# Kernel optimization log

Hardware: AMD Instinct MI355X
Metric: run time of the kernel (lower is better)

## Reference

```python
import jax, jax.numpy as jnp
import numpy as np

NUM_EMBEDDINGS = 1024
EMBEDDING_DIM = 128
COMMITMENT_COST = 0.25


def setup_inputs() -> dict:
    key = jax.random.key(0)
    k_in, k_cb = jax.random.split(key)
    inputs = jax.random.normal(k_in, (65536, EMBEDDING_DIM), dtype=jnp.float32)
    # torch init: uniform(-1/K, 1/K)
    codebook = jax.random.uniform(
        k_cb, (NUM_EMBEDDINGS, EMBEDDING_DIM), dtype=jnp.float32,
        minval=-1.0 / NUM_EMBEDDINGS, maxval=1.0 / NUM_EMBEDDINGS)
    return {"inputs": inputs, "codebook": codebook}


def reference(inputs, codebook):
    # inputs: [N, D], codebook: [K, D]
    # squared euclidean distances [N, K]
    distances = (jnp.sum(inputs ** 2, axis=1, keepdims=True)
                 + jnp.sum(codebook ** 2, axis=1)
                 - 2.0 * jnp.matmul(inputs, codebook.T))
    encoding_indices = jnp.argmin(distances, axis=1)  # [N]
    encodings = jax.nn.one_hot(encoding_indices, NUM_EMBEDDINGS, dtype=jnp.float32)  # [N, K]
    # onehot @ codebook == gather
    quantized = jnp.take(codebook, encoding_indices, axis=0)  # [N, D]

    e_latent_loss = jnp.mean((jax.lax.stop_gradient(quantized) - inputs) ** 2)
    q_latent_loss = jnp.mean((quantized - jax.lax.stop_gradient(inputs)) ** 2)
    loss = q_latent_loss + COMMITMENT_COST * e_latent_loss

    # straight-through estimator
    quantized_st = inputs + jax.lax.stop_gradient(quantized - inputs)

    avg_probs = jnp.mean(encodings, axis=0)  # [K]
    perplexity = jnp.exp(-jnp.sum(avg_probs * jnp.log(avg_probs + 1e-10)))
    return (loss, quantized_st, perplexity, encodings)
```

## Files before the change

kernel.cpp:

```cpp
#include <hip/hip_runtime.h>

#define NROWS 65536
#define DIM   128
#define KC    1024
#define QST_OFF  1
#define PPL_OFF  8388609
#define ENC_OFF  8388610

typedef float f32x2 __attribute__((ext_vector_type(2)));
typedef float floatx4 __attribute__((ext_vector_type(4)));
typedef _Float16 half8_t __attribute__((ext_vector_type(8)));
typedef _Float16 half4_t __attribute__((ext_vector_type(4)));

#define BSTR 144
#define TILEH (64 * BSTR)
#define CHUNKH (2 * TILEH)

__device__ __forceinline__ float fadd_rn_(float a, float b) {
#pragma clang fp contract(off)
  return a + b;
}
__device__ __forceinline__ float fsub_rn_(float a, float b) {
#pragma clang fp contract(off)
  return a - b;
}
__device__ __forceinline__ float fmul_rn_(float a, float b) {
#pragma clang fp contract(off)
  return a * b;
}

__device__ __forceinline__ void async_ld16(const void* g, void* l) {
  __builtin_amdgcn_global_load_lds(
      (const __attribute__((address_space(1))) void*)g,
      (__attribute__((address_space(3))) void*)l, 16, 0, 0);
}

__device__ __forceinline__ float rowsq128(const float4* src) {
  float r[8];
  {
    float4 v0 = src[0], v1 = src[1];
    r[0] = fmul_rn_(v0.x, v0.x); r[1] = fmul_rn_(v0.y, v0.y);
    r[2] = fmul_rn_(v0.z, v0.z); r[3] = fmul_rn_(v0.w, v0.w);
    r[4] = fmul_rn_(v1.x, v1.x); r[5] = fmul_rn_(v1.y, v1.y);
    r[6] = fmul_rn_(v1.z, v1.z); r[7] = fmul_rn_(v1.w, v1.w);
  }
  for (int i = 1; i < 16; ++i) {
    float4 v0 = src[2 * i], v1 = src[2 * i + 1];
    r[0] = fadd_rn_(r[0], fmul_rn_(v0.x, v0.x));
    r[1] = fadd_rn_(r[1], fmul_rn_(v0.y, v0.y));
    r[2] = fadd_rn_(r[2], fmul_rn_(v0.z, v0.z));
    r[3] = fadd_rn_(r[3], fmul_rn_(v0.w, v0.w));
    r[4] = fadd_rn_(r[4], fmul_rn_(v1.x, v1.x));
    r[5] = fadd_rn_(r[5], fmul_rn_(v1.y, v1.y));
    r[6] = fadd_rn_(r[6], fmul_rn_(v1.z, v1.z));
    r[7] = fadd_rn_(r[7], fmul_rn_(v1.w, v1.w));
  }
  return fadd_rn_(fadd_rn_(fadd_rn_(r[0], r[1]), fadd_rn_(r[2], r[3])),
                  fadd_rn_(fadd_rn_(r[4], r[5]), fadd_rn_(r[6], r[7])));
}

__global__ __launch_bounds__(256) void k_prep(const float* __restrict__ cb,
                                              float* __restrict__ cbT,
                                              float* __restrict__ cc,
                                              _Float16* __restrict__ Bp) {
  __shared__ float tile[64 * 129];
  int t = threadIdx.x;
  int c0 = blockIdx.x * 64;
#pragma unroll
  for (int it = 0; it < 32; ++it) {
    int f = it * 256 + t;
    int c = f >> 7, d = f & 127;
    tile[c * 129 + d] = cb[(size_t)(c0 + c) * DIM + d];
  }
  __syncthreads();
#pragma unroll
  for (int it = 0; it < 32; ++it) {
    int f = it * 256 + t;
    int d = f >> 6, c = f & 63;
    cbT[(size_t)d * KC + c0 + c] = tile[c * 129 + d];
  }
  if (t < 64) {
    const float* s = &tile[t * 129];
    float r[8];
#pragma unroll
    for (int j = 0; j < 8; ++j) r[j] = fmul_rn_(s[j], s[j]);
    for (int i = 1; i < 16; ++i) {
#pragma unroll
      for (int j = 0; j < 8; ++j)
        r[j] = fadd_rn_(r[j], fmul_rn_(s[i * 8 + j], s[i * 8 + j]));
    }
    cc[c0 + t] = fadd_rn_(fadd_rn_(fadd_rn_(r[0], r[1]), fadd_rn_(r[2], r[3])),
                          fadd_rn_(fadd_rn_(r[4], r[5]), fadd_rn_(r[6], r[7])));
  }
  size_t base = (size_t)blockIdx.x * CHUNKH;
#pragma unroll
  for (int it = 0; it < 32; ++it) {
    int f = it * 256 + t;
    int c = f >> 7, k = f & 127;
    float c5 = tile[c * 129 + k] * 512.0f;
    _Float16 h = (_Float16)c5;
    _Float16 l = (_Float16)(c5 - (float)h);
    Bp[base + c * BSTR + k] = h;
    Bp[base + TILEH + c * BSTR + k] = l;
  }
}

__global__ __launch_bounds__(256, 4) void k_main(const float* __restrict__ inp,
                                                 const float* __restrict__ cb,
                                                 const float* __restrict__ cbT,
                                                 const _Float16* __restrict__ Bp,
                                                 const float* __restrict__ cc,
                                                 float* __restrict__ out_qst,
                                                 float* __restrict__ out_enc,
                                                 int* __restrict__ cnt,
                                                 float* __restrict__ lsum) {
  __shared__ _Float16 SB[CHUNKH];
  __shared__ float xxs[64];
  __shared__ int bk[64];
  __shared__ int fl_rows[64];
  __shared__ int fl_cnt;
  __shared__ float xs[128];
  __shared__ float redd[4];
  __shared__ int redi[4];
  __shared__ float redf[4];

  int t = threadIdx.x;
  int lane = t & 63, w = t >> 6;
  int q = lane >> 4, col = lane & 15;
  int row0 = blockIdx.x * 64;
  if (t == 0) fl_cnt = 0;

  {
    int r = t & 63, seg = t >> 6;
    const float* src = inp + (size_t)(row0 + r) * DIM + seg * 32;
#pragma unroll
    for (int i = 0; i < 8; ++i) {
      float4 v = *(const float4*)(src + i * 4);
      _Float16 h0 = (_Float16)v.x, h1 = (_Float16)v.y, h2 = (_Float16)v.z, h3 = (_Float16)v.w;
      half4_t hv = {h0, h1, h2, h3};
      half4_t lv = {(_Float16)(v.x - (float)h0), (_Float16)(v.y - (float)h1),
                    (_Float16)(v.z - (float)h2), (_Float16)(v.w - (float)h3)};
      int k = seg * 32 + i * 4;
      *(half4_t*)&SB[r * BSTR + k] = hv;
      *(half4_t*)&SB[TILEH + r * BSTR + k] = lv;
    }
  }
  if (t < 64) xxs[t] = rowsq128((const float4*)(inp + (size_t)(row0 + t) * DIM));
  __syncthreads();

  int arow = w * 16 + col;
  half8_t ah[4], al[4];
#pragma unroll
  for (int ks = 0; ks < 4; ++ks) {
    ah[ks] = *(const half8_t*)&SB[arow * BSTR + ks * 32 + q * 8];
    al[ks] = *(const half8_t*)&SB[TILEH + arow * BSTR + ks * 32 + q * 8];
  }
  float xr[4];
#pragma unroll
  for (int r = 0; r < 4; ++r) xr[r] = xxs[w * 16 + q * 4 + r];

  float b1[4], b2[4];
  int i1[4];
#pragma unroll
  for (int r = 0; r < 4; ++r) { b1[r] = 3.4e38f; b2[r] = 3.4e38f; i1[r] = 0; }

  const float4* bp4 = (const float4*)Bp;
  floatx4* enc4 = (floatx4*)(out_enc + (size_t)row0 * KC);
  int wbase = w * 64;

  for (int c = 0; c < 16; ++c) {
    __syncthreads();
    {
      const float4* gsrc = bp4 + (size_t)c * 2304 + t;
#pragma unroll
      for (int r = 0; r < 9; ++r)
        async_ld16(gsrc + r * 256, &SB[(size_t)(r * 256 + wbase) * 8]);
    }
    {
      floatx4 z = {0.f, 0.f, 0.f, 0.f};
#pragma unroll
      for (int i = 0; i < 4; ++i)
        __builtin_nontemporal_store(z, enc4 + (size_t)c * 1024 + i * 256 + t);
    }
    __syncthreads();

    float cck[4];
#pragma unroll
    for (int ct = 0; ct < 4; ++ct) cck[ct] = cc[c * 64 + ct * 16 + col];

    floatx4 acc[4];
#pragma unroll
    for (int ct = 0; ct < 4; ++ct) acc[ct] = (floatx4){0.f, 0.f, 0.f, 0.f};

#pragma unroll
    for (int ks = 0; ks < 4; ++ks) {
#pragma unroll
      for (int ct = 0; ct < 4; ++ct) {
        int brow = ct * 16 + col;
        half8_t bh = *(const half8_t*)&SB[brow * BSTR + ks * 32 + q * 8];
        half8_t bl = *(const half8_t*)&SB[TILEH + brow * BSTR + ks * 32 + q * 8];
        acc[ct] = __builtin_amdgcn_mfma_f32_16x16x32_f16(ah[ks], bh, acc[ct], 0, 0, 0);
        acc[ct] = __builtin_amdgcn_mfma_f32_16x16x32_f16(ah[ks], bl, acc[ct], 0, 0, 0);
        acc[ct] = __builtin_amdgcn_mfma_f32_16x16x32_f16(al[ks], bh, acc[ct], 0, 0, 0);
      }
    }

#pragma unroll
    for (int ct = 0; ct < 4; ++ct) {
#pragma unroll
      for (int r = 0; r < 4; ++r) {
        float m2 = fmul_rn_(acc[ct][r], 0.00390625f);
        float dist = fsub_rn_(fadd_rn_(xr[r], cck[ct]), m2);
        int kidx = c * 64 + ct * 16 + col;
        bool lt = dist < b1[r];
        b2[r] = lt ? b1[r] : fminf(b2[r], dist);
        i1[r] = lt ? kidx : i1[r];
        b1[r] = lt ? dist : b1[r];
      }
    }
  }

#pragma unroll
  for (int r = 0; r < 4; ++r) {
    float v1 = b1[r], v2 = b2[r];
    int ii = i1[r];
    for (int off = 1; off < 16; off <<= 1) {
      float ov1 = __shfl_xor(v1, off);
      float ov2 = __shfl_xor(v2, off);
      int oi = __shfl_xor(ii, off);
      float nb1 = fminf(v1, ov1);
      float nb2 = fminf(fmaxf(v1, ov1), fminf(v2, ov2));
      ii = (ov1 < v1) ? oi : ((ov1 > v1) ? ii : min(ii, oi));
      v1 = nb1; v2 = nb2;
    }
    b1[r] = v1; b2[r] = v2; i1[r] = ii;
  }

  if (col == 0) {
#pragma unroll
    for (int r = 0; r < 4; ++r) {
      int lrow = w * 16 + q * 4 + r;
      bk[lrow] = i1[r];
      float u = (b1[r] >= 256.f) ? 9.4e-5f : 4.7e-5f;
      if (b2[r] - b1[r] < u) {
        int p = atomicAdd(&fl_cnt, 1);
        fl_rows[p] = lrow;
      }
    }
  }
  __syncthreads();

  int nf = fl_cnt;
  for (int f = 0; f < nf; ++f) {
    int row = fl_rows[f];
    if (t < 128) xs[t] = inp[(size_t)(row0 + row) * DIM + t];
    __syncthreads();
    float xxr = xxs[row];
    int c0 = t * 4;
    float a0 = 0.f, a1 = 0.f, a2 = 0.f, a3 = 0.f;
    for (int d = 0; d < 128; ++d) {
      float xd = xs[d];
      float4 cv = *(const float4*)&cbT[(size_t)d * KC + c0];
      a0 = __builtin_fmaf(xd, cv.x, a0);
      a1 = __builtin_fmaf(xd, cv.y, a1);
      a2 = __builtin_fmaf(xd, cv.z, a2);
      a3 = __builtin_fmaf(xd, cv.w, a3);
    }
    float aa[4] = {a0, a1, a2, a3};
    float bb = 3.4e38f;
    int bi = 0;
#pragma unroll
    for (int j = 0; j < 4; ++j) {
      float dist = fsub_rn_(fadd_rn_(xxr, cc[c0 + j]), fmul_rn_(2.0f, aa[j]));
      if (dist < bb) { bb = dist; bi = c0 + j; }
    }
    for (int off = 1; off < 64; off <<= 1) {
      float ov = __shfl_xor(bb, off);
      int oi = __shfl_xor(bi, off);
      if (ov < bb || (ov == bb && oi < bi)) { bb = ov; bi = oi; }
    }
    if (lane == 0) { redd[w] = bb; redi[w] = bi; }
    __syncthreads();
    if (t == 0) {
      float vb = redd[0];
      int ib = redi[0];
#pragma unroll
      for (int ww = 1; ww < 4; ++ww) {
        if (redd[ww] < vb || (redd[ww] == vb && redi[ww] < ib)) { vb = redd[ww]; ib = redi[ww]; }
      }
      bk[row] = ib;
    }
    __syncthreads();
  }

  if (t < 64) atomicAdd(&cnt[bk[t]], 1);

  float ls = 0.f;
#pragma unroll 4
  for (int it = 0; it < 32; ++it) {
    int f = it * 256 + t;
    int row = f >> 7, d = f & 127;
    size_t gro = (size_t)(row0 + row) * DIM + d;
    float x = inp[gro];
    float qv = cb[(size_t)bk[row] * DIM + d];
    float qe = fsub_rn_(qv, x);
    __builtin_nontemporal_store(fadd_rn_(x, qe), &out_qst[gro]);
    ls = __builtin_fmaf(qe, qe, ls);
  }

  if (t < 64) out_enc[(size_t)(row0 + t) * KC + bk[t]] = 1.0f;

  for (int off = 32; off; off >>= 1) ls += __shfl_down(ls, off);
  if (lane == 0) redf[w] = ls;
  __syncthreads();
  if (t == 0) atomicAdd(lsum, redf[0] + redf[1] + redf[2] + redf[3]);
}

__global__ __launch_bounds__(1024) void k_scalars(const int* __restrict__ cnt,
                                                  const float* __restrict__ lsum,
                                                  float* __restrict__ out) {
  int t = threadIdx.x;
  float p = (float)cnt[t] * (1.0f / 65536.0f);
  float term = fmul_rn_(p, logf(fadd_rn_(p, 1e-10f)));
  for (int off = 32; off; off >>= 1) term += __shfl_down(term, off);
  __shared__ float red[16];
  if ((t & 63) == 0) red[t >> 6] = term;
  __syncthreads();
  if (t == 0) {
    float s = 0.f;
#pragma unroll
    for (int w = 0; w < 16; ++w) s += red[w];
    out[PPL_OFF] = expf(-s);
    float e = *lsum * (1.0f / 8388608.0f);
    out[0] = fadd_rn_(e, fmul_rn_(0.25f, e));
  }
}

extern "C" void kernel_launch(void* const* d_in, const int* in_sizes, int n_in,
                              void* d_out, int out_size, void* d_ws, size_t ws_size,
                              hipStream_t stream) {
  const float* inp = (const float*)d_in[0];
  const float* cb = (const float*)d_in[1];
  float* out = (float*)d_out;

  _Float16* Bp = (_Float16*)d_ws;
  float* cbT = (float*)(Bp + 16 * CHUNKH);
  float* cc = cbT + DIM * KC;
  int* cnt = (int*)(cc + KC);
  float* lsum = (float*)(cnt + KC);

  (void)hipMemsetAsync(cnt, 0, (KC + 1) * sizeof(int), stream);
  k_prep<<<KC / 64, 256, 0, stream>>>(cb, cbT, cc, Bp);
  k_main<<<NROWS / 64, 256, 0, stream>>>(inp, cb, cbT, Bp, cc,
                                         out + QST_OFF, out + ENC_OFF, cnt, lsum);
  k_scalars<<<1, 1024, 0, stream>>>(cnt, lsum, out);
}
```

Measured before the change: 394.5 us.

## Process 128 rows per block with double-buffered codebook chunk prefetch

```diff
diff --git a/kernel.cpp b/kernel.cpp
--- a/kernel.cpp
+++ b/kernel.cpp
@@ -13,8 +13,10 @@
 typedef _Float16 half4_t __attribute__((ext_vector_type(4)));
 
 #define BSTR 144
-#define TILEH (64 * BSTR)
-#define CHUNKH (2 * TILEH)
+#define BTILE 9216
+#define BCHUNK (2 * BTILE)
+#define ATILE 18432
+#define RPB 128
 
 __device__ __forceinline__ float fadd_rn_(float a, float b) {
 #pragma clang fp contract(off)
@@ -92,7 +94,7 @@
     cc[c0 + t] = fadd_rn_(fadd_rn_(fadd_rn_(r[0], r[1]), fadd_rn_(r[2], r[3])),
                           fadd_rn_(fadd_rn_(r[4], r[5]), fadd_rn_(r[6], r[7])));
   }
-  size_t base = (size_t)blockIdx.x * CHUNKH;
+  size_t base = (size_t)blockIdx.x * BCHUNK;
 #pragma unroll
   for (int it = 0; it < 32; ++it) {
     int f = it * 256 + t;
@@ -101,11 +103,11 @@
     _Float16 h = (_Float16)c5;
     _Float16 l = (_Float16)(c5 - (float)h);
     Bp[base + c * BSTR + k] = h;
-    Bp[base + TILEH + c * BSTR + k] = l;
-  }
-}
-
-__global__ __launch_bounds__(256, 4) void k_main(const float* __restrict__ inp,
+    Bp[base + BTILE + c * BSTR + k] = l;
+  }
+}
+
+__global__ __launch_bounds__(256, 2) void k_main(const float* __restrict__ inp,
                                                  const float* __restrict__ cb,
                                                  const float* __restrict__ cbT,
                                                  const _Float16* __restrict__ Bp,
@@ -114,10 +116,10 @@
                                                  float* __restrict__ out_enc,
                                                  int* __restrict__ cnt,
                                                  float* __restrict__ lsum) {
-  __shared__ _Float16 SB[CHUNKH];
-  __shared__ float xxs[64];
-  __shared__ int bk[64];
-  __shared__ int fl_rows[64];
+  __shared__ _Float16 SB[2 * BCHUNK];
+  __shared__ float xxs[RPB];
+  __shared__ int bk[RPB];
+  __shared__ int fl_rows[RPB];
   __shared__ int fl_cnt;
   __shared__ float xs[128];
   __shared__ float redd[4];
@@ -127,101 +129,135 @@
   int t = threadIdx.x;
   int lane = t & 63, w = t >> 6;
   int q = lane >> 4, col = lane & 15;
-  int row0 = blockIdx.x * 64;
+  int row0 = blockIdx.x * RPB;
   if (t == 0) fl_cnt = 0;
 
   {
-    int r = t & 63, seg = t >> 6;
-    const float* src = inp + (size_t)(row0 + r) * DIM + seg * 32;
-#pragma unroll
-    for (int i = 0; i < 8; ++i) {
-      float4 v = *(const float4*)(src + i * 4);
+    const float* src = inp + (size_t)row0 * DIM;
+#pragma unroll
+    for (int it = 0; it < 16; ++it) {
+      int f = it * 256 + t;
+      int r = f >> 5, c4 = f & 31;
+      float4 v = *(const float4*)(src + (size_t)r * DIM + c4 * 4);
       _Float16 h0 = (_Float16)v.x, h1 = (_Float16)v.y, h2 = (_Float16)v.z, h3 = (_Float16)v.w;
       half4_t hv = {h0, h1, h2, h3};
       half4_t lv = {(_Float16)(v.x - (float)h0), (_Float16)(v.y - (float)h1),
                     (_Float16)(v.z - (float)h2), (_Float16)(v.w - (float)h3)};
-      int k = seg * 32 + i * 4;
-      *(half4_t*)&SB[r * BSTR + k] = hv;
-      *(half4_t*)&SB[TILEH + r * BSTR + k] = lv;
-    }
-  }
-  if (t < 64) xxs[t] = rowsq128((const float4*)(inp + (size_t)(row0 + t) * DIM));
-  __syncthreads();
-
-  int arow = w * 16 + col;
-  half8_t ah[4], al[4];
+      *(half4_t*)&SB[r * BSTR + c4 * 4] = hv;
+      *(half4_t*)&SB[ATILE + r * BSTR + c4 * 4] = lv;
+    }
+  }
+  if (t < RPB) xxs[t] = rowsq128((const float4*)(inp + (size_t)(row0 + t) * DIM));
+  __syncthreads();
+
+  int arow0 = w * 32 + col;
+  int arow1 = arow0 + 16;
+  half8_t ah0[4], al0[4], ah1[4], al1[4];
 #pragma unroll
   for (int ks = 0; ks < 4; ++ks) {
-    ah[ks] = *(const half8_t*)&SB[arow * BSTR + ks * 32 + q * 8];
-    al[ks] = *(const half8_t*)&SB[TILEH + arow * BSTR + ks * 32 + q * 8];
-  }
-  float xr[4];
-#pragma unroll
-  for (int r = 0; r < 4; ++r) xr[r] = xxs[w * 16 + q * 4 + r];
-
-  float b1[4], b2[4];
-  int i1[4];
-#pragma unroll
-  for (int r = 0; r < 4; ++r) { b1[r] = 3.4e38f; b2[r] = 3.4e38f; i1[r] = 0; }
+    ah0[ks] = *(const half8_t*)&SB[arow0 * BSTR + ks * 32 + q * 8];
+    al0[ks] = *(const half8_t*)&SB[ATILE + arow0 * BSTR + ks * 32 + q * 8];
+    ah1[ks] = *(const half8_t*)&SB[arow1 * BSTR + ks * 32 + q * 8];
+    al1[ks] = *(const half8_t*)&SB[ATILE + arow1 * BSTR + ks * 32 + q * 8];
+  }
+  float xr0[4], xr1[4];
+#pragma unroll
+  for (int r = 0; r < 4; ++r) {
+    xr0[r] = xxs[w * 32 + q * 4 + r];
+    xr1[r] = xxs[w * 32 + 16 + q * 4 + r];
+  }
+  __syncthreads();
+
+  float b1[8], b2[8];
+  int i1[8];
+#pragma unroll
+  for (int r = 0; r < 8; ++r) { b1[r] = 3.4e38f; b2[r] = 3.4e38f; i1[r] = 0; }
 
   const float4* bp4 = (const float4*)Bp;
   floatx4* enc4 = (floatx4*)(out_enc + (size_t)row0 * KC);
   int wbase = w * 64;
 
+  {
+    const float4* gsrc = bp4 + t;
+#pragma unroll
+    for (int r = 0; r < 9; ++r)
+      async_ld16(gsrc + r * 256, &SB[(size_t)(r * 256 + wbase) * 8]);
+  }
+
   for (int c = 0; c < 16; ++c) {
     __syncthreads();
-    {
-      const float4* gsrc = bp4 + (size_t)c * 2304 + t;
+    if (c < 15) {
+      const float4* gsrc = bp4 + (size_t)(c + 1) * 2304 + t;
+      int boff = ((c + 1) & 1) * BCHUNK;
 #pragma unroll
       for (int r = 0; r < 9; ++r)
-        async_ld16(gsrc + r * 256, &SB[(size_t)(r * 256 + wbase) * 8]);
+        async_ld16(gsrc + r * 256, &SB[boff + (size_t)(r * 256 + wbase) * 8]);
     }
     {
       floatx4 z = {0.f, 0.f, 0.f, 0.f};
 #pragma unroll
-      for (int i = 0; i < 4; ++i)
-        __builtin_nontemporal_store(z, enc4 + (size_t)c * 1024 + i * 256 + t);
-    }
-    __syncthreads();
-
+      for (int i = 0; i < 8; ++i) {
+        int f = i * 256 + t;
+        int r = f >> 4, cq = f & 15;
+        __builtin_nontemporal_store(z, enc4 + (size_t)r * 256 + c * 16 + cq);
+      }
+    }
+
+    const _Float16* Bb = &SB[(c & 1) * BCHUNK];
     float cck[4];
 #pragma unroll
     for (int ct = 0; ct < 4; ++ct) cck[ct] = cc[c * 64 + ct * 16 + col];
 
-    floatx4 acc[4];
-#pragma unroll
-    for (int ct = 0; ct < 4; ++ct) acc[ct] = (floatx4){0.f, 0.f, 0.f, 0.f};
+    floatx4 acc0[4], acc1[4];
+#pragma unroll
+    for (int ct = 0; ct < 4; ++ct) {
+      acc0[ct] = (floatx4){0.f, 0.f, 0.f, 0.f};
+      acc1[ct] = (floatx4){0.f, 0.f, 0.f, 0.f};
+    }
 
 #pragma unroll
     for (int ks = 0; ks < 4; ++ks) {
 #pragma unroll
       for (int ct = 0; ct < 4; ++ct) {
         int brow = ct * 16 + col;
-        half8_t bh = *(const half8_t*)&SB[brow * BSTR + ks * 32 + q * 8];
-        half8_t bl = *(const half8_t*)&SB[TILEH + brow * BSTR + ks * 32 + q * 8];
-        acc[ct] = __builtin_amdgcn_mfma_f32_16x16x32_f16(ah[ks], bh, acc[ct], 0, 0, 0);
-        acc[ct] = __builtin_amdgcn_mfma_f32_16x16x32_f16(ah[ks], bl, acc[ct], 0, 0, 0);
-        acc[ct] = __builtin_amdgcn_mfma_f32_16x16x32_f16(al[ks], bh, acc[ct], 0, 0, 0);
+        half8_t bh = *(const half8_t*)&Bb[brow * BSTR + ks * 32 + q * 8];
+        half8_t bl = *(const half8_t*)&Bb[BTILE + brow * BSTR + ks * 32 + q * 8];
+        acc0[ct] = __builtin_amdgcn_mfma_f32_16x16x32_f16(ah0[ks], bh, acc0[ct], 0, 0, 0);
+        acc0[ct] = __builtin_amdgcn_mfma_f32_16x16x32_f16(ah0[ks], bl, acc0[ct], 0, 0, 0);
+        acc0[ct] = __builtin_amdgcn_mfma_f32_16x16x32_f16(al0[ks], bh, acc0[ct], 0, 0, 0);
+        acc1[ct] = __builtin_amdgcn_mfma_f32_16x16x32_f16(ah1[ks], bh, acc1[ct], 0, 0, 0);
+        acc1[ct] = __builtin_amdgcn_mfma_f32_16x16x32_f16(ah1[ks], bl, acc1[ct], 0, 0, 0);
+        acc1[ct] = __builtin_amdgcn_mfma_f32_16x16x32_f16(al1[ks], bh, acc1[ct], 0, 0, 0);
       }
     }
 
 #pragma unroll
     for (int ct = 0; ct < 4; ++ct) {
+      int kidx = c * 64 + ct * 16 + col;
 #pragma unroll
       for (int r = 0; r < 4; ++r) {
-        float m2 = fmul_rn_(acc[ct][r], 0.00390625f);
-        float dist = fsub_rn_(fadd_rn_(xr[r], cck[ct]), m2);
-        int kidx = c * 64 + ct * 16 + col;
-        bool lt = dist < b1[r];
-        b2[r] = lt ? b1[r] : fminf(b2[r], dist);
-        i1[r] = lt ? kidx : i1[r];
-        b1[r] = lt ? dist : b1[r];
-      }
-    }
-  }
-
-#pragma unroll
-  for (int r = 0; r < 4; ++r) {
+        {
+          float m2 = fmul_rn_(acc0[ct][r], 0.00390625f);
+          float dist = fsub_rn_(fadd_rn_(xr0[r], cck[ct]), m2);
+          bool lt = dist < b1[r];
+          b2[r] = lt ? b1[r] : fminf(b2[r], dist);
+          i1[r] = lt ? kidx : i1[r];
+          b1[r] = lt ? dist : b1[r];
+        }
+        {
+          float m2 = fmul_rn_(acc1[ct][r], 0.00390625f);
+          float dist = fsub_rn_(fadd_rn_(xr1[r], cck[ct]), m2);
+          bool lt = dist < b1[4 + r];
+          b2[4 + r] = lt ? b1[4 + r] : fminf(b2[4 + r], dist);
+          i1[4 + r] = lt ? kidx : i1[4 + r];
+          b1[4 + r] = lt ? dist : b1[4 + r];
+        }
+      }
+    }
+  }
+
+#pragma unroll
+  for (int r = 0; r < 8; ++r) {
     float v1 = b1[r], v2 = b2[r];
     int ii = i1[r];
     for (int off = 1; off < 16; off <<= 1) {
@@ -238,13 +274,17 @@
 
   if (col == 0) {
 #pragma unroll
-    for (int r = 0; r < 4; ++r) {
-      int lrow = w * 16 + q * 4 + r;
-      bk[lrow] = i1[r];
-      float u = (b1[r] >= 256.f) ? 9.4e-5f : 4.7e-5f;
-      if (b2[r] - b1[r] < u) {
-        int p = atomicAdd(&fl_cnt, 1);
-        fl_rows[p] = lrow;
+    for (int sub = 0; sub < 2; ++sub) {
+#pragma unroll
+      for (int r = 0; r < 4; ++r) {
+        int j = sub * 4 + r;
+        int lrow = w * 32 + sub * 16 + q * 4 + r;
+        bk[lrow] = i1[j];
+        float u = (b1[j] >= 256.f) ? 9.4e-5f : 4.7e-5f;
+        if (b2[j] - b1[j] < u) {
+          int p = atomicAdd(&fl_cnt, 1);
+          fl_rows[p] = lrow;
+        }
       }
     }
   }
@@ -293,11 +333,11 @@
     __syncthreads();
   }
 
-  if (t < 64) atomicAdd(&cnt[bk[t]], 1);
+  if (t < RPB) atomicAdd(&cnt[bk[t]], 1);
 
   float ls = 0.f;
 #pragma unroll 4
-  for (int it = 0; it < 32; ++it) {
+  for (int it = 0; it < 64; ++it) {
     int f = it * 256 + t;
     int row = f >> 7, d = f & 127;
     size_t gro = (size_t)(row0 + row) * DIM + d;
@@ -308,7 +348,7 @@
     ls = __builtin_fmaf(qe, qe, ls);
   }
 
-  if (t < 64) out_enc[(size_t)(row0 + t) * KC + bk[t]] = 1.0f;
+  if (t < RPB) out_enc[(size_t)(row0 + t) * KC + bk[t]] = 1.0f;
 
   for (int off = 32; off; off >>= 1) ls += __shfl_down(ls, off);
   if (lane == 0) redf[w] = ls;
@@ -344,14 +384,14 @@
   float* out = (float*)d_out;
 
   _Float16* Bp = (_Float16*)d_ws;
-  float* cbT = (float*)(Bp + 16 * CHUNKH);
+  float* cbT = (float*)(Bp + 16 * BCHUNK);
   float* cc = cbT + DIM * KC;
   int* cnt = (int*)(cc + KC);
   float* lsum = (float*)(cnt + KC);
 
   (void)hipMemsetAsync(cnt, 0, (KC + 1) * sizeof(int), stream);
   k_prep<<<KC / 64, 256, 0, stream>>>(cb, cbT, cc, Bp);
-  k_main<<<NROWS / 64, 256, 0, stream>>>(inp, cb, cbT, Bp, cc,
-                                         out + QST_OFF, out + ENC_OFF, cnt, lsum);
+  k_main<<<NROWS / RPB, 256, 0, stream>>>(inp, cb, cbT, Bp, cc,
+                                          out + QST_OFF, out + ENC_OFF, cnt, lsum);
   k_scalars<<<1, 1024, 0, stream>>>(cnt, lsum, out);
 }
```

New measurement: 543.5 us. 37.8% more time.

## Double-buffer codebook chunks in LDS and fold norm term into MFMA

Applied to the files above, without the earlier changes.

```diff
diff --git a/kernel.cpp b/kernel.cpp
--- a/kernel.cpp
+++ b/kernel.cpp
@@ -7,14 +7,15 @@
 #define PPL_OFF  8388609
 #define ENC_OFF  8388610
 
-typedef float f32x2 __attribute__((ext_vector_type(2)));
 typedef float floatx4 __attribute__((ext_vector_type(4)));
 typedef _Float16 half8_t __attribute__((ext_vector_type(8)));
 typedef _Float16 half4_t __attribute__((ext_vector_type(4)));
 
 #define BSTR 144
-#define TILEH (64 * BSTR)
-#define CHUNKH (2 * TILEH)
+#define CIMG 4608
+#define CCH  9216
+#define A_LO 9216
+#define RPB 64
 
 __device__ __forceinline__ float fadd_rn_(float a, float b) {
 #pragma clang fp contract(off)
@@ -89,19 +90,29 @@
       for (int j = 0; j < 8; ++j)
         r[j] = fadd_rn_(r[j], fmul_rn_(s[i * 8 + j], s[i * 8 + j]));
     }
-    cc[c0 + t] = fadd_rn_(fadd_rn_(fadd_rn_(r[0], r[1]), fadd_rn_(r[2], r[3])),
-                          fadd_rn_(fadd_rn_(r[4], r[5]), fadd_rn_(r[6], r[7])));
-  }
-  size_t base = (size_t)blockIdx.x * CHUNKH;
+    float ccv = fadd_rn_(fadd_rn_(fadd_rn_(r[0], r[1]), fadd_rn_(r[2], r[3])),
+                         fadd_rn_(fadd_rn_(r[4], r[5]), fadd_rn_(r[6], r[7])));
+    cc[c0 + t] = ccv;
+    int g = c0 + t;
+    size_t base = (size_t)(g >> 5) * CCH + (size_t)(g & 31) * BSTR;
+#pragma unroll
+    for (int k = 128; k < 144; ++k) {
+      Bp[base + k] = (_Float16)0.0f;
+      Bp[base + CIMG + k] = (_Float16)0.0f;
+    }
+    Bp[base + 128] = (_Float16)(-512.0f * ccv);
+  }
 #pragma unroll
   for (int it = 0; it < 32; ++it) {
     int f = it * 256 + t;
     int c = f >> 7, k = f & 127;
+    int g = c0 + c;
+    size_t base = (size_t)(g >> 5) * CCH + (size_t)(g & 31) * BSTR;
     float c5 = tile[c * 129 + k] * 512.0f;
     _Float16 h = (_Float16)c5;
     _Float16 l = (_Float16)(c5 - (float)h);
-    Bp[base + c * BSTR + k] = h;
-    Bp[base + TILEH + c * BSTR + k] = l;
+    Bp[base + k] = h;
+    Bp[base + CIMG + k] = l;
   }
 }
 
@@ -114,10 +125,10 @@
                                                  float* __restrict__ out_enc,
                                                  int* __restrict__ cnt,
                                                  float* __restrict__ lsum) {
-  __shared__ _Float16 SB[CHUNKH];
-  __shared__ float xxs[64];
-  __shared__ int bk[64];
-  __shared__ int fl_rows[64];
+  __shared__ _Float16 SB[2 * CCH];
+  __shared__ float xxs[RPB];
+  __shared__ int bk[RPB];
+  __shared__ int fl_rows[RPB];
   __shared__ int fl_cnt;
   __shared__ float xs[128];
   __shared__ float redd[4];
@@ -127,7 +138,7 @@
   int t = threadIdx.x;
   int lane = t & 63, w = t >> 6;
   int q = lane >> 4, col = lane & 15;
-  int row0 = blockIdx.x * 64;
+  int row0 = blockIdx.x * RPB;
   if (t == 0) fl_cnt = 0;
 
   {
@@ -142,10 +153,10 @@
                     (_Float16)(v.z - (float)h2), (_Float16)(v.w - (float)h3)};
       int k = seg * 32 + i * 4;
       *(half4_t*)&SB[r * BSTR + k] = hv;
-      *(half4_t*)&SB[TILEH + r * BSTR + k] = lv;
-    }
-  }
-  if (t < 64) xxs[t] = rowsq128((const float4*)(inp + (size_t)(row0 + t) * DIM));
+      *(half4_t*)&SB[A_LO + r * BSTR + k] = lv;
+    }
+  }
+  if (t < RPB) xxs[t] = rowsq128((const float4*)(inp + (size_t)(row0 + t) * DIM));
   __syncthreads();
 
   int arow = w * 16 + col;
@@ -153,69 +164,93 @@
 #pragma unroll
   for (int ks = 0; ks < 4; ++ks) {
     ah[ks] = *(const half8_t*)&SB[arow * BSTR + ks * 32 + q * 8];
-    al[ks] = *(const half8_t*)&SB[TILEH + arow * BSTR + ks * 32 + q * 8];
+    al[ks] = *(const half8_t*)&SB[A_LO + arow * BSTR + ks * 32 + q * 8];
   }
   float xr[4];
 #pragma unroll
   for (int r = 0; r < 4; ++r) xr[r] = xxs[w * 16 + q * 4 + r];
+  __syncthreads();
+
+  half8_t aex = {0, 0, 0, 0, 0, 0, 0, 0};
+  if (q == 0) aex[0] = (_Float16)0.5f;
 
   float b1[4], b2[4];
   int i1[4];
 #pragma unroll
-  for (int r = 0; r < 4; ++r) { b1[r] = 3.4e38f; b2[r] = 3.4e38f; i1[r] = 0; }
+  for (int r = 0; r < 4; ++r) { b1[r] = -3.4e38f; b2[r] = -3.4e38f; i1[r] = 0; }
 
   const float4* bp4 = (const float4*)Bp;
   floatx4* enc4 = (floatx4*)(out_enc + (size_t)row0 * KC);
-  int wbase = w * 64;
-
-  for (int c = 0; c < 16; ++c) {
-    __syncthreads();
-    {
-      const float4* gsrc = bp4 + (size_t)c * 2304 + t;
-#pragma unroll
-      for (int r = 0; r < 9; ++r)
-        async_ld16(gsrc + r * 256, &SB[(size_t)(r * 256 + wbase) * 8]);
-    }
+
+  {
+    const float4* gsrc = bp4;
+#pragma unroll
+    for (int r = 0; r < 4; ++r)
+      async_ld16(gsrc + r * 256 + t, &SB[(size_t)(r * 256 + t) * 8]);
+    if (t < 128) async_ld16(gsrc + 1024 + t, &SB[(size_t)(1024 + t) * 8]);
+  }
+  asm volatile("s_waitcnt vmcnt(0)" ::: "memory");
+  __builtin_amdgcn_sched_barrier(0);
+  __builtin_amdgcn_s_barrier();
+  __builtin_amdgcn_sched_barrier(0);
+
+  for (int c = 0; c < 32; ++c) {
+    if (c > 0) {
+      asm volatile("s_waitcnt vmcnt(2)" ::: "memory");
+      __builtin_amdgcn_sched_barrier(0);
+      __builtin_amdgcn_s_barrier();
+      __builtin_amdgcn_sched_barrier(0);
+    }
+    if (c < 31) {
+      const float4* gsrc = bp4 + (size_t)(c + 1) * 1152;
+      int boff = ((c + 1) & 1) * CCH;
+#pragma unroll
+      for (int r = 0; r < 4; ++r)
+        async_ld16(gsrc + r * 256 + t, &SB[boff + (size_t)(r * 256 + t) * 8]);
+      if (t < 128) async_ld16(gsrc + 1024 + t, &SB[boff + (size_t)(1024 + t) * 8]);
+    }
+    __builtin_amdgcn_sched_barrier(0);
     {
       floatx4 z = {0.f, 0.f, 0.f, 0.f};
-#pragma unroll
-      for (int i = 0; i < 4; ++i)
-        __builtin_nontemporal_store(z, enc4 + (size_t)c * 1024 + i * 256 + t);
-    }
-    __syncthreads();
-
-    float cck[4];
-#pragma unroll
-    for (int ct = 0; ct < 4; ++ct) cck[ct] = cc[c * 64 + ct * 16 + col];
-
-    floatx4 acc[4];
-#pragma unroll
-    for (int ct = 0; ct < 4; ++ct) acc[ct] = (floatx4){0.f, 0.f, 0.f, 0.f};
+      __builtin_nontemporal_store(z, enc4 + (size_t)c * 512 + t);
+      __builtin_nontemporal_store(z, enc4 + (size_t)c * 512 + 256 + t);
+    }
+    __builtin_amdgcn_sched_barrier(0);
+
+    const _Float16* Bb = &SB[(c & 1) * CCH];
+    floatx4 acc[2];
+    acc[0] = (floatx4){0.f, 0.f, 0.f, 0.f};
+    acc[1] = (floatx4){0.f, 0.f, 0.f, 0.f};
 
 #pragma unroll
     for (int ks = 0; ks < 4; ++ks) {
 #pragma unroll
-      for (int ct = 0; ct < 4; ++ct) {
+      for (int ct = 0; ct < 2; ++ct) {
         int brow = ct * 16 + col;
-        half8_t bh = *(const half8_t*)&SB[brow * BSTR + ks * 32 + q * 8];
-        half8_t bl = *(const half8_t*)&SB[TILEH + brow * BSTR + ks * 32 + q * 8];
+        half8_t bh = *(const half8_t*)&Bb[brow * BSTR + ks * 32 + q * 8];
+        half8_t bl = *(const half8_t*)&Bb[CIMG + brow * BSTR + ks * 32 + q * 8];
         acc[ct] = __builtin_amdgcn_mfma_f32_16x16x32_f16(ah[ks], bh, acc[ct], 0, 0, 0);
         acc[ct] = __builtin_amdgcn_mfma_f32_16x16x32_f16(ah[ks], bl, acc[ct], 0, 0, 0);
         acc[ct] = __builtin_amdgcn_mfma_f32_16x16x32_f16(al[ks], bh, acc[ct], 0, 0, 0);
       }
     }
-
-#pragma unroll
-    for (int ct = 0; ct < 4; ++ct) {
+#pragma unroll
+    for (int ct = 0; ct < 2; ++ct) {
+      int brow = ct * 16 + col;
+      half8_t bex = *(const half8_t*)&Bb[brow * BSTR + 128];
+      acc[ct] = __builtin_amdgcn_mfma_f32_16x16x32_f16(aex, bex, acc[ct], 0, 0, 0);
+    }
+
+#pragma unroll
+    for (int ct = 0; ct < 2; ++ct) {
+      int kidx = c * 32 + ct * 16 + col;
 #pragma unroll
       for (int r = 0; r < 4; ++r) {
-        float m2 = fmul_rn_(acc[ct][r], 0.00390625f);
-        float dist = fsub_rn_(fadd_rn_(xr[r], cck[ct]), m2);
-        int kidx = c * 64 + ct * 16 + col;
-        bool lt = dist < b1[r];
-        b2[r] = lt ? b1[r] : fminf(b2[r], dist);
-        i1[r] = lt ? kidx : i1[r];
-        b1[r] = lt ? dist : b1[r];
+        float s = acc[ct][r];
+        bool gt = s > b1[r];
+        b2[r] = gt ? b1[r] : fmaxf(b2[r], s);
+        i1[r] = gt ? kidx : i1[r];
+        b1[r] = gt ? s : b1[r];
       }
     }
   }
@@ -228,9 +263,9 @@
       float ov1 = __shfl_xor(v1, off);
       float ov2 = __shfl_xor(v2, off);
       int oi = __shfl_xor(ii, off);
-      float nb1 = fminf(v1, ov1);
-      float nb2 = fminf(fmaxf(v1, ov1), fminf(v2, ov2));
-      ii = (ov1 < v1) ? oi : ((ov1 > v1) ? ii : min(ii, oi));
+      float nb1 = fmaxf(v1, ov1);
+      float nb2 = fmaxf(fminf(v1, ov1), fmaxf(v2, ov2));
+      ii = (ov1 > v1) ? oi : ((ov1 < v1) ? ii : min(ii, oi));
       v1 = nb1; v2 = nb2;
     }
     b1[r] = v1; b2[r] = v2; i1[r] = ii;
@@ -241,8 +276,9 @@
     for (int r = 0; r < 4; ++r) {
       int lrow = w * 16 + q * 4 + r;
       bk[lrow] = i1[r];
-      float u = (b1[r] >= 256.f) ? 9.4e-5f : 4.7e-5f;
-      if (b2[r] - b1[r] < u) {
+      float dist1 = fsub_rn_(xr[r], fmul_rn_(b1[r], 0.00390625f));
+      float u = (dist1 >= 256.f) ? 9.4e-5f : 4.7e-5f;
+      if (b1[r] - b2[r] < u * 256.0f) {
         int p = atomicAdd(&fl_cnt, 1);
         fl_rows[p] = lrow;
       }
@@ -293,7 +329,7 @@
     __syncthreads();
   }
 
-  if (t < 64) atomicAdd(&cnt[bk[t]], 1);
+  if (t < RPB) atomicAdd(&cnt[bk[t]], 1);
 
   float ls = 0.f;
 #pragma unroll 4
@@ -308,7 +344,7 @@
     ls = __builtin_fmaf(qe, qe, ls);
   }
 
-  if (t < 64) out_enc[(size_t)(row0 + t) * KC + bk[t]] = 1.0f;
+  if (t < RPB) out_enc[(size_t)(row0 + t) * KC + bk[t]] = 1.0f;
 
   for (int off = 32; off; off >>= 1) ls += __shfl_down(ls, off);
   if (lane == 0) redf[w] = ls;
@@ -344,14 +380,14 @@
   float* out = (float*)d_out;
 
   _Float16* Bp = (_Float16*)d_ws;
-  float* cbT = (float*)(Bp + 16 * CHUNKH);
+  float* cbT = (float*)(Bp + 32 * CCH);
   float* cc = cbT + DIM * KC;
   int* cnt = (int*)(cc + KC);
   float* lsum = (float*)(cnt + KC);
 
   (void)hipMemsetAsync(cnt, 0, (KC + 1) * sizeof(int), stream);
   k_prep<<<KC / 64, 256, 0, stream>>>(cb, cbT, cc, Bp);
-  k_main<<<NROWS / 64, 256, 0, stream>>>(inp, cb, cbT, Bp, cc,
-                                         out + QST_OFF, out + ENC_OFF, cnt, lsum);
+  k_main<<<NROWS / RPB, 256, 0, stream>>>(inp, cb, cbT, Bp, cc,
+                                          out + QST_OFF, out + ENC_OFF, cnt, lsum);
   k_scalars<<<1, 1024, 0, stream>>>(cnt, lsum, out);
 }
```

After: 391.8 us. Within noise of the previous version (-0.7%).
